# Kernel tuning notes

Hardware: AMD Instinct MI355X
Metric: run time of the kernel (lower is better)

## Reference

```python
import jax, jax.numpy as jnp
import numpy as np

B, S, D, H = 32, 1024, 192, 8
DH = D // H  # 24


def setup_inputs() -> dict:
    key = jax.random.key(0)
    ks = jax.random.split(key, 8)
    s_in = 1.0 / np.sqrt(D)
    return {
        "x": jax.random.normal(ks[0], (B, S, D), dtype=jnp.float32),
        "mask": jax.random.randint(ks[1], (B, S), 0, 2).astype(bool),
        "Wq": jax.random.normal(ks[2], (H, D, DH), dtype=jnp.float32) * s_in,
        "bq": jnp.zeros((H, DH), dtype=jnp.float32),
        "Wk": jax.random.normal(ks[3], (H, D, DH), dtype=jnp.float32) * s_in,
        "bk": jnp.zeros((H, DH), dtype=jnp.float32),
        "Wv": jax.random.normal(ks[4], (H, D, DH), dtype=jnp.float32) * s_in,
        "bv": jnp.zeros((H, DH), dtype=jnp.float32),
        "Wo": jax.random.normal(ks[5], (D, D), dtype=jnp.float32) * s_in,
        "bo": jnp.zeros((D,), dtype=jnp.float32),
    }


def reference(x, mask, Wq, bq, Wk, bk, Wv, bv, Wo, bo):
    # Batched per-head projections: [B,S,D] x [H,D,DH] -> [B,H,S,DH]
    q = jnp.einsum("bsd,hde->bhse", x, Wq) + bq[None, :, None, :]
    k = jnp.einsum("bsd,hde->bhse", x, Wk) + bk[None, :, None, :]
    v = jnp.einsum("bsd,hde->bhse", x, Wv) + bv[None, :, None, :]
    scale = 1.0 / np.sqrt(DH).astype(np.float32)
    scores = jnp.einsum("bhse,bhte->bhst", q, k) * scale  # [B,H,S,S]
    # mask [B,S] broadcast over heads and query positions (masked_fill with -1e9)
    scores = jnp.where(mask[:, None, None, :], scores, -1e9)
    weights = jax.nn.softmax(scores, axis=-1)
    out = jnp.einsum("bhst,bhte->bhse", weights, v)  # [B,H,S,DH]
    # concat heads along last dim -> [B,S,D]
    out = out.transpose(0, 2, 1, 3).reshape(B, S, D)
    return out @ Wo + bo
```

## Files before the change

### kernel.cpp

```cpp
#include <hip/hip_runtime.h>

typedef __attribute__((ext_vector_type(8))) short short8;
typedef __attribute__((ext_vector_type(4))) float f32x4;
typedef __attribute__((ext_vector_type(16))) float f32x16;
typedef __attribute__((ext_vector_type(2))) unsigned uint2v;
typedef __attribute__((ext_vector_type(4))) unsigned uint4v;

#define MFMA16(a,b,c) __builtin_amdgcn_mfma_f32_16x16x32_bf16((a),(b),(c),0,0,0)
#define MFMA32(a,b,c) __builtin_amdgcn_mfma_f32_32x32x16_bf16((a),(b),(c),0,0,0)

#define BB 32
#define SS 1024
#define DD 192
#define HH 8
#define DHP 32

#define SCALE_Q 0.294468266742895f

__device__ __forceinline__ short nb(float f) {
    __bf16 h = (__bf16)f;
    return __builtin_bit_cast(short, h);
}
__device__ __forceinline__ float bf2f(short s) {
    union { unsigned u; float f; } v; v.u = ((unsigned)(unsigned short)s) << 16;
    return v.f;
}
__device__ __forceinline__ unsigned pk2(float a, float b) {
    unsigned short lo = __builtin_bit_cast(unsigned short, (__bf16)a);
    unsigned short hi = __builtin_bit_cast(unsigned short, (__bf16)b);
    return (unsigned)lo | ((unsigned)hi << 16);
}

__global__ __launch_bounds__(256) void prep_kernel(
    const float* __restrict__ Wq, const float* __restrict__ Wk, const float* __restrict__ Wv,
    const float* __restrict__ Wo,
    short* __restrict__ WqF, short* __restrict__ WkF, short* __restrict__ WvF,
    short* __restrict__ WoFh, short* __restrict__ WoFl)
{
    int idx = blockIdx.x * 256 + threadIdx.x;
    const int NWX   = 3 * HH * DHP * DD;
    const int NWO   = DD * DD;
    if (idx < NWX) {
        int j = idx;
        int mat = j / (HH * DHP * DD);
        int jj  = j % (HH * DHP * DD);
        int h   = jj / (DHP * DD);
        int rem = jj % (DHP * DD);
        int e   = rem / DD;
        int d   = rem % DD;
        const float* W = (mat == 0) ? Wq : (mat == 1) ? Wk : Wv;
        short* WF      = (mat == 0) ? WqF : (mat == 1) ? WkF : WvF;
        float val = (e < 24) ? W[(h * DD + d) * 24 + e] : 0.f;
        int nt = e & 1, cc = e >> 1;
        int kk = d >> 5, g = (d >> 3) & 3, ee = d & 7;
        WF[(size_t)((((h*2+nt)*6 + kk)*64) + g*16 + cc)*8 + ee] = nb(val);
    } else if (idx < NWX + NWO) {
        int j = idx - NWX;
        int n = j / DD, k = j % DD;
        float f = Wo[k * DD + n];
        short hi = nb(f);
        int nn = n >> 4, cc = n & 15;
        int kk = k >> 5, g = (k >> 3) & 3, ee = k & 7;
        size_t addr = (size_t)(((nn*6 + kk)*64) + g*16 + cc)*8 + ee;
        WoFh[addr] = hi;
        WoFl[addr] = nb(f - bf2f(hi));
    }
}

__global__ __launch_bounds__(256) void xprep_kernel(
    const float* __restrict__ x, short* __restrict__ xF)
{
    __shared__ short lds[64][200];
    int t = threadIdx.x;
    int r0 = blockIdx.x * 64;

    #pragma unroll
    for (int i = 0; i < 12; i++) {
        int idx = i * 256 + t;
        int row = idx / 48;
        int colf = (idx % 48) * 4;
        float4 f = *(const float4*)(x + ((size_t)(r0 + row)) * DD + colf);
        lds[row][colf + 0] = nb(f.x);
        lds[row][colf + 1] = nb(f.y);
        lds[row][colf + 2] = nb(f.z);
        lds[row][colf + 3] = nb(f.w);
    }
    __syncthreads();

    int w = t >> 6, lane = t & 63, c = lane & 15, g = lane >> 4;
    int br = blockIdx.x * 4 + w;
    short* outb = xF + (size_t)br * 6 * 512;
    #pragma unroll
    for (int kk = 0; kk < 6; kk++) {
        short8 o = *(const short8*)&lds[w * 16 + c][kk * 32 + g * 8];
        *(short8*)(outb + kk * 512 + (size_t)lane * 8) = o;
    }
}

__global__ __launch_bounds__(1024) void scan_kernel(
    const void* __restrict__ mask_raw,
    float* __restrict__ maskf, int* __restrict__ fwd, int* __restrict__ cnt)
{
    int b = blockIdx.x, t = threadIdx.x;
    int lane = t & 63, wv = t >> 6;
    int idx = b * SS + t;

    const unsigned* mw = (const unsigned*)mask_raw;
    bool all01 = true, allf = true;
    #pragma unroll
    for (int i = 0; i < 16; i++) {
        unsigned w = mw[i];
        all01 = all01 && (w <= 1u);
        allf  = allf  && (w == 0u || w == 0x3F800000u);
    }
    bool m;
    if (all01)      m = (mw[idx] != 0u);
    else if (allf)  m = (((const float*)mask_raw)[idx] != 0.f);
    else            m = (((const unsigned char*)mask_raw)[idx] != 0);
    maskf[idx] = m ? 1.f : 0.f;

    unsigned long long bal = __ballot(m);
    int preU  = __popcll(bal & ((1ull << lane) - 1ull));
    int waveU = __popcll(bal);
    __shared__ int wsu[16];
    if (lane == 0) wsu[wv] = waveU;
    __syncthreads();
    int waveOffU = 0, totalU = 0;
    #pragma unroll
    for (int i = 0; i < 16; i++) {
        int v = wsu[i];
        if (i < wv) waveOffU += v;
        totalU += v;
    }
    int posU = waveOffU + preU;
    int posM = totalU + (wv * 64 - waveOffU) + (lane - preU);
    fwd[b * SS + (m ? posU : posM)] = t;
    if (t == 0) cnt[b] = totalU;
}

__global__ __launch_bounds__(256) void proj_kernel(
    const short* __restrict__ xF,
    const float* __restrict__ bq, const float* __restrict__ bk, const float* __restrict__ bv,
    const short* __restrict__ WqF, const short* __restrict__ WkF, const short* __restrict__ WvF,
    const float* __restrict__ maskf,
    short* __restrict__ Q, short* __restrict__ Kc, short* __restrict__ Vc)
{
    int tid = threadIdx.x;
    int lane = tid & 63, w = tid >> 6;
    int c = lane & 15, g = lane >> 4;
    int r0 = blockIdx.x * 64 + w * 16;
    int h0 = blockIdx.y * 2;

    int b_ = r0 >> 10;
    int s0 = (r0 & 1023) + g * 4;

    short8 a[6];
    const short* xfb = xF + (size_t)(r0 >> 4) * 6 * 512 + (size_t)lane * 8;
    #pragma unroll
    for (int kk = 0; kk < 6; kk++)
        a[kk] = *(const short8*)(xfb + kk * 512);

    float mrow[4];
    #pragma unroll
    for (int r = 0; r < 4; r++) mrow[r] = maskf[b_ * SS + s0 + r];

    #pragma unroll
    for (int hh = 0; hh < 2; hh++) {
        int h = h0 + hh;
        int bh = b_ * HH + h;
        #pragma unroll
        for (int mat = 0; mat < 3; mat++) {
            const short* WF   = (mat==0)?WqF:(mat==1)?WkF:WvF;
            const float* bias = (mat==0)?bq:(mat==1)?bk:bv;

            f32x4 acc0 = {0.f,0.f,0.f,0.f};
            f32x4 acc1 = {0.f,0.f,0.f,0.f};
            const short* Wp0 = WF + (size_t)((h*2+0)*6) * 512 + lane * 8;
            const short* Wp1 = WF + (size_t)((h*2+1)*6) * 512 + lane * 8;
            #pragma unroll
            for (int kk = 0; kk < 6; kk++) {
                short8 b0 = *(const short8*)(Wp0 + kk * 512);
                short8 b1 = *(const short8*)(Wp1 + kk * 512);
                acc0 = MFMA16(a[kk], b0, acc0);
                acc1 = MFMA16(a[kk], b1, acc1);
            }
            float bv0 = 0.f, bv1 = 0.f;
            if (2*c < 24) {
                float2 bb = *(const float2*)(bias + h * 24 + 2 * c);
                bv0 = bb.x; bv1 = bb.y;
            }

            if (mat == 0) {
                #pragma unroll
                for (int r = 0; r < 4; r++) {
                    float v0 = (acc0[r] + bv0) * SCALE_Q;
                    float v1 = (c == 15) ? 1.0f : (acc1[r] + bv1) * SCALE_Q;
                    *(unsigned*)(Q + ((size_t)bh * SS + s0 + r) * DHP + 2*c) = pk2(v0, v1);
                }
            } else if (mat == 1) {
                #pragma unroll
                for (int r = 0; r < 4; r++) {
                    float v0 = acc0[r] + bv0;
                    float v1 = (c == 15) ? ((mrow[r] != 0.f) ? 0.f : -1e30f)
                                         : (acc1[r] + bv1);
                    *(unsigned*)(Kc + ((size_t)bh * SS + s0 + r) * DHP + 2*c) = pk2(v0, v1);
                }
            } else {
                #pragma unroll
                for (int r = 0; r < 4; r++) {
                    float v0 = (c == 12) ? 1.0f : (acc0[r] + bv0);
                    float v1 = acc1[r] + bv1;
                    *(unsigned*)(Vc + ((size_t)bh * SS + s0 + r) * DHP + 2*c) = pk2(v0, v1);
                }
            }
        }
    }
}

__global__ __launch_bounds__(256) void kvprep_kernel(
    const short* __restrict__ Kc, const short* __restrict__ Vc,
    const int* __restrict__ fwd, const int* __restrict__ cnt,
    short* __restrict__ KF, short* __restrict__ VF)
{
    int bh = blockIdx.x, c4 = blockIdx.y;
    int b = bh >> 3;
    int nt32 = ((cnt[b] + 31) >> 5) << 5;
    int row0 = c4 * 128;
    if (row0 >= nt32) return;

    __shared__ short lds[128][40];
    int t = threadIdx.x;
    int srow[2];

    #pragma unroll
    for (int p = 0; p < 2; p++) {
        int j = p * 64 + (t >> 2);
        int part = t & 3;
        int s = fwd[b * SS + row0 + j];
        srow[p] = s;
        *(short8*)&lds[j][part * 8] =
            *(const short8*)(Kc + ((size_t)bh * SS + s) * DHP + part * 8);
    }
    __syncthreads();

    int tile_l = t >> 6, L = t & 63, l31 = L & 31, hi = L >> 5;
    short* kf0 = KF + (size_t)bh * SS * DHP + (size_t)(row0 / 32 + tile_l) * 1024;
    #pragma unroll
    for (int i = 0; i < 2; i++) {
        short8 o = *(const short8*)&lds[tile_l * 32 + l31][i * 16 + hi * 8];
        *(short8*)(kf0 + i * 512 + (size_t)L * 8) = o;
    }
    __syncthreads();

    #pragma unroll
    for (int p = 0; p < 2; p++) {
        int j = p * 64 + (t >> 2);
        int part = t & 3;
        *(short8*)&lds[j][part * 8] =
            *(const short8*)(Vc + ((size_t)bh * SS + srow[p]) * DHP + part * 8);
    }
    __syncthreads();

    short* vf0 = VF + (size_t)bh * SS * DHP + (size_t)(row0 / 32 + tile_l) * 1024;
    #pragma unroll
    for (int i = 0; i < 2; i++) {
        short8 o;
        #pragma unroll
        for (int j2 = 0; j2 < 8; j2++)
            o[j2] = lds[tile_l * 32 + i * 16 + hi * 8 + j2][l31];
        *(short8*)(vf0 + i * 512 + (size_t)L * 8) = o;
    }
}

__device__ __forceinline__ void fproc(const f32x16& S, f32x16& acc,
                                      short8 v0, short8 v1)
{
    float p[16];
    #pragma unroll
    for (int r = 0; r < 16; r++) p[r] = __builtin_amdgcn_exp2f(S[r]);

    unsigned c01 = pk2(p[0],  p[1]);
    unsigned c23 = pk2(p[2],  p[3]);
    unsigned c45 = pk2(p[4],  p[5]);
    unsigned c67 = pk2(p[6],  p[7]);
    unsigned c89 = pk2(p[8],  p[9]);
    unsigned cab = pk2(p[10], p[11]);
    unsigned ccd = pk2(p[12], p[13]);
    unsigned cef = pk2(p[14], p[15]);

    uint2v s0 = __builtin_amdgcn_permlane32_swap(c01, c45, false, false);
    uint2v s1 = __builtin_amdgcn_permlane32_swap(c23, c67, false, false);
    uint2v s2 = __builtin_amdgcn_permlane32_swap(c89, ccd, false, false);
    uint2v s3 = __builtin_amdgcn_permlane32_swap(cab, cef, false, false);

    uint4v w0v = { s0.x, s1.x, s0.y, s1.y };
    uint4v w1v = { s2.x, s3.x, s2.y, s3.y };
    short8 pa0 = __builtin_bit_cast(short8, w0v);
    short8 pa1 = __builtin_bit_cast(short8, w1v);

    acc = MFMA32(pa0, v0, acc);
    acc = MFMA32(pa1, v1, acc);
}

__global__ __launch_bounds__(256, 2) void flash_kernel(
    const short* __restrict__ Q, const short* __restrict__ KF, const short* __restrict__ VF,
    const int* __restrict__ cnt, short* __restrict__ Af)
{
    __shared__ float llds[4][4][32];

    int idx = blockIdx.x;
    int bh = idx & 255;
    int qb = idx >> 8;
    int b = bh >> 3, h = bh & 7;

    int tid = threadIdx.x;
    int lane = tid & 63, w = tid >> 6;
    int l31 = lane & 31;
    int hi = lane >> 5;

    int nt = (cnt[b] + 31) >> 5;

    int qr0 = qb * 512 + w * 32;

    short8 qf[4][2];
    #pragma unroll
    for (int cc = 0; cc < 4; cc++) {
        const short* Qp = Q + ((size_t)bh * SS + qr0 + cc * 128 + l31) * DHP + hi * 8;
        qf[cc][0] = *(const short8*)Qp;
        qf[cc][1] = *(const short8*)(Qp + 16);
    }

    const short* Kp = KF + (size_t)bh * SS * DHP + (size_t)lane * 8;
    const short* Vp = VF + (size_t)bh * SS * DHP + (size_t)lane * 8;

    f32x16 acc[4], Z16;
    #pragma unroll
    for (int r = 0; r < 16; r++) {
        acc[0][r] = 0.f; acc[1][r] = 0.f; acc[2][r] = 0.f; acc[3][r] = 0.f;
        Z16[r] = 0.f;
    }

    short8 k0 = *(const short8*)(Kp);
    short8 k1 = *(const short8*)(Kp + 512);
    short8 v0 = *(const short8*)(Vp);
    short8 v1 = *(const short8*)(Vp + 512);

    for (int kt = 0; kt < nt; kt++) {
        Kp += 1024;
        Vp += 1024;
        short8 nk0 = *(const short8*)(Kp);
        short8 nk1 = *(const short8*)(Kp + 512);
        short8 nv0 = *(const short8*)(Vp);
        short8 nv1 = *(const short8*)(Vp + 512);

        #pragma unroll
        for (int cc = 0; cc < 4; cc++) {
            f32x16 S = MFMA32(k0, qf[cc][0], Z16);
            S = MFMA32(k1, qf[cc][1], S);
            fproc(S, acc[cc], v0, v1);
        }

        k0 = nk0; k1 = nk1; v0 = nv0; v1 = nv1;
    }

    if (l31 == 24) {
        #pragma unroll
        for (int cc = 0; cc < 4; cc++) {
            #pragma unroll
            for (int r = 0; r < 16; r++) {
                int row = (r & 3) + 8 * (r >> 2) + 4 * hi;
                llds[w][cc][row] = __builtin_amdgcn_rcpf(acc[cc][r]);
            }
        }
    }
    __builtin_amdgcn_wave_barrier();

    if (l31 < 24) {
        int d = h * 24 + l31;
        size_t fcol = (size_t)((d >> 5) * 4 + ((d >> 3) & 3)) * 128 + (d & 7);
        #pragma unroll
        for (int cc = 0; cc < 4; cc++) {
            int grp = (b * SS + qr0 + cc * 128) >> 4;
            short* op = Af + (size_t)grp * 3072 + fcol;
            #pragma unroll
            for (int r = 0; r < 16; r++) {
                int row = (r & 3) + 8 * (r >> 2) + 4 * hi;
                size_t off = (size_t)(r >> 3) * 3072 + (size_t)(row & 15) * 8;
                op[off] = nb(acc[cc][r] * llds[w][cc][row]);
            }
        }
    }
}

__global__ __launch_bounds__(256) void final_kernel(
    const short* __restrict__ Af,
    const short* __restrict__ WoFh, const short* __restrict__ WoFl,
    const float* __restrict__ bo, float* __restrict__ out)
{
    int tid = threadIdx.x;
    int lane = tid & 63, w = tid >> 6;
    int c = lane & 15, g = lane >> 4;
    int r0 = blockIdx.x * 64 + w * 16;
    int n0 = blockIdx.y * 3;

    short8 a[6];
    #pragma unroll
    for (int kk = 0; kk < 6; kk++)
        a[kk] = *(const short8*)(Af + ((size_t)(r0 >> 4) * 24 + kk*4 + g) * 128 + c * 8);

    f32x4 acc[3];
    #pragma unroll
    for (int n = 0; n < 3; n++) acc[n] = (f32x4){0.f,0.f,0.f,0.f};

    #pragma unroll
    for (int kk = 0; kk < 6; kk++) {
        #pragma unroll
        for (int n = 0; n < 3; n++) {
            const short* bh_p = WoFh + (size_t)((n0+n)*6 + kk) * 512 + lane * 8;
            const short* bl_p = WoFl + (size_t)((n0+n)*6 + kk) * 512 + lane * 8;
            short8 bh = *(const short8*)bh_p;
            short8 bl = *(const short8*)bl_p;
            acc[n] = MFMA16(a[kk], bh, acc[n]);
            acc[n] = MFMA16(a[kk], bl, acc[n]);
        }
    }

    #pragma unroll
    for (int n = 0; n < 3; n++) {
        int col = (n0+n)*16 + c;
        float bv = bo[col];
        #pragma unroll
        for (int r = 0; r < 4; r++) {
            out[(size_t)(r0 + g*4 + r) * DD + col] = acc[n][r] + bv;
        }
    }
}

extern "C" void kernel_launch(void* const* d_in, const int* in_sizes, int n_in,
                              void* d_out, int out_size, void* d_ws, size_t ws_size,
                              hipStream_t stream)
{
    const float* x    = (const float*)d_in[0];
    const void*  mask = d_in[1];
    const float* Wq   = (const float*)d_in[2];
    const float* bq   = (const float*)d_in[3];
    const float* Wk   = (const float*)d_in[4];
    const float* bk   = (const float*)d_in[5];
    const float* Wv   = (const float*)d_in[6];
    const float* bv   = (const float*)d_in[7];
    const float* Wo   = (const float*)d_in[8];
    const float* bo   = (const float*)d_in[9];
    float* out = (float*)d_out;

    char* ws = (char*)d_ws;
    size_t off = 0;
    float* maskf = (float*)(ws + off); off += (size_t)BB*SS*4;
    short* Q     = (short*)(ws + off); off += (size_t)BB*HH*SS*DHP*2;
    short* Kc    = (short*)(ws + off); off += (size_t)BB*HH*SS*DHP*2;
    short* Vc    = (short*)(ws + off); off += (size_t)BB*HH*SS*DHP*2;
    short* KF    = (short*)(ws + off); off += (size_t)BB*HH*SS*DHP*2;
    short* VF    = (short*)(ws + off); off += (size_t)BB*HH*SS*DHP*2;
    short* xF    = (short*)(ws + off); off += (size_t)BB*SS*DD*2;
    short* WqF   = (short*)(ws + off); off += (size_t)HH*DHP*DD*2;
    short* WkF   = (short*)(ws + off); off += (size_t)HH*DHP*DD*2;
    short* WvF   = (short*)(ws + off); off += (size_t)HH*DHP*DD*2;
    short* WoFh  = (short*)(ws + off); off += (size_t)DD*DD*2;
    short* WoFl  = (short*)(ws + off); off += (size_t)DD*DD*2;
    int*   fwd   = (int*)  (ws + off); off += (size_t)BB*SS*4;
    int*   cnt   = (int*)  (ws + off); off += 256;

    short* Af = Kc;

    prep_kernel<<<dim3(720), dim3(256), 0, stream>>>(
        Wq, Wk, Wv, Wo, WqF, WkF, WvF, WoFh, WoFl);
    xprep_kernel<<<dim3(512), dim3(256), 0, stream>>>(x, xF);
    scan_kernel<<<dim3(BB), dim3(1024), 0, stream>>>(mask, maskf, fwd, cnt);
    proj_kernel<<<dim3(512, 4), dim3(256), 0, stream>>>(
        xF, bq, bk, bv, WqF, WkF, WvF, maskf, Q, Kc, Vc);
    kvprep_kernel<<<dim3(256, 8), dim3(256), 0, stream>>>(
        Kc, Vc, fwd, cnt, KF, VF);
    flash_kernel<<<dim3(512), dim3(256), 0, stream>>>(
        Q, KF, VF, cnt, Af);
    final_kernel<<<dim3(512, 4), dim3(256), 0, stream>>>(
        Af, WoFh, WoFl, bo, out);
}
```

Baseline: 100.8 us.

## Merge prep kernels into one launch, drop Wo split-bf16, widen proj grid

Combines the weight prep, x conversion and mask scan kernels into a single setup kernel dispatched by block index, which removes two launches. The mask scan now uses 256 threads handling four positions each, with a shuffle-based prefix sum. The output projection drops the low-order bf16 correction term for Wo, halving its MFMAs and weight loads at some cost in accuracy. The projection kernel now assigns one head per block across 8 grid columns instead of two heads per block, giving more parallelism.

```diff
diff --git a/kernel.cpp b/kernel.cpp
--- a/kernel.cpp
+++ b/kernel.cpp
@@ -31,111 +31,116 @@
     return (unsigned)lo | ((unsigned)hi << 16);
 }
 
-__global__ __launch_bounds__(256) void prep_kernel(
+#define NBLK_PREP 720
+#define NBLK_XPREP 512
+__global__ __launch_bounds__(256) void setup_kernel(
     const float* __restrict__ Wq, const float* __restrict__ Wk, const float* __restrict__ Wv,
-    const float* __restrict__ Wo,
+    const float* __restrict__ Wo, const float* __restrict__ x, const void* __restrict__ mask_raw,
     short* __restrict__ WqF, short* __restrict__ WkF, short* __restrict__ WvF,
-    short* __restrict__ WoFh, short* __restrict__ WoFl)
-{
-    int idx = blockIdx.x * 256 + threadIdx.x;
-    const int NWX   = 3 * HH * DHP * DD;
-    const int NWO   = DD * DD;
-    if (idx < NWX) {
-        int j = idx;
-        int mat = j / (HH * DHP * DD);
-        int jj  = j % (HH * DHP * DD);
-        int h   = jj / (DHP * DD);
-        int rem = jj % (DHP * DD);
-        int e   = rem / DD;
-        int d   = rem % DD;
-        const float* W = (mat == 0) ? Wq : (mat == 1) ? Wk : Wv;
-        short* WF      = (mat == 0) ? WqF : (mat == 1) ? WkF : WvF;
-        float val = (e < 24) ? W[(h * DD + d) * 24 + e] : 0.f;
-        int nt = e & 1, cc = e >> 1;
-        int kk = d >> 5, g = (d >> 3) & 3, ee = d & 7;
-        WF[(size_t)((((h*2+nt)*6 + kk)*64) + g*16 + cc)*8 + ee] = nb(val);
-    } else if (idx < NWX + NWO) {
-        int j = idx - NWX;
-        int n = j / DD, k = j % DD;
-        float f = Wo[k * DD + n];
-        short hi = nb(f);
-        int nn = n >> 4, cc = n & 15;
-        int kk = k >> 5, g = (k >> 3) & 3, ee = k & 7;
-        size_t addr = (size_t)(((nn*6 + kk)*64) + g*16 + cc)*8 + ee;
-        WoFh[addr] = hi;
-        WoFl[addr] = nb(f - bf2f(hi));
-    }
-}
-
-__global__ __launch_bounds__(256) void xprep_kernel(
-    const float* __restrict__ x, short* __restrict__ xF)
+    short* __restrict__ WoFh, short* __restrict__ xF,
+    float* __restrict__ maskf, int* __restrict__ fwd, int* __restrict__ cnt)
 {
     __shared__ short lds[64][200];
+    int bid = blockIdx.x;
     int t = threadIdx.x;
-    int r0 = blockIdx.x * 64;
-
-    #pragma unroll
-    for (int i = 0; i < 12; i++) {
-        int idx = i * 256 + t;
-        int row = idx / 48;
-        int colf = (idx % 48) * 4;
-        float4 f = *(const float4*)(x + ((size_t)(r0 + row)) * DD + colf);
-        lds[row][colf + 0] = nb(f.x);
-        lds[row][colf + 1] = nb(f.y);
-        lds[row][colf + 2] = nb(f.z);
-        lds[row][colf + 3] = nb(f.w);
-    }
-    __syncthreads();
-
-    int w = t >> 6, lane = t & 63, c = lane & 15, g = lane >> 4;
-    int br = blockIdx.x * 4 + w;
-    short* outb = xF + (size_t)br * 6 * 512;
-    #pragma unroll
-    for (int kk = 0; kk < 6; kk++) {
-        short8 o = *(const short8*)&lds[w * 16 + c][kk * 32 + g * 8];
-        *(short8*)(outb + kk * 512 + (size_t)lane * 8) = o;
-    }
-}
-
-__global__ __launch_bounds__(1024) void scan_kernel(
-    const void* __restrict__ mask_raw,
-    float* __restrict__ maskf, int* __restrict__ fwd, int* __restrict__ cnt)
-{
-    int b = blockIdx.x, t = threadIdx.x;
-    int lane = t & 63, wv = t >> 6;
-    int idx = b * SS + t;
-
-    const unsigned* mw = (const unsigned*)mask_raw;
-    bool all01 = true, allf = true;
-    #pragma unroll
-    for (int i = 0; i < 16; i++) {
-        unsigned w = mw[i];
-        all01 = all01 && (w <= 1u);
-        allf  = allf  && (w == 0u || w == 0x3F800000u);
-    }
-    bool m;
-    if (all01)      m = (mw[idx] != 0u);
-    else if (allf)  m = (((const float*)mask_raw)[idx] != 0.f);
-    else            m = (((const unsigned char*)mask_raw)[idx] != 0);
-    maskf[idx] = m ? 1.f : 0.f;
-
-    unsigned long long bal = __ballot(m);
-    int preU  = __popcll(bal & ((1ull << lane) - 1ull));
-    int waveU = __popcll(bal);
-    __shared__ int wsu[16];
-    if (lane == 0) wsu[wv] = waveU;
-    __syncthreads();
-    int waveOffU = 0, totalU = 0;
-    #pragma unroll
-    for (int i = 0; i < 16; i++) {
-        int v = wsu[i];
-        if (i < wv) waveOffU += v;
-        totalU += v;
-    }
-    int posU = waveOffU + preU;
-    int posM = totalU + (wv * 64 - waveOffU) + (lane - preU);
-    fwd[b * SS + (m ? posU : posM)] = t;
-    if (t == 0) cnt[b] = totalU;
+
+    if (bid < NBLK_PREP) {
+        int idx = bid * 256 + t;
+        const int NWX = 3 * HH * DHP * DD;
+        const int NWO = DD * DD;
+        if (idx < NWX) {
+            int mat = idx / (HH * DHP * DD);
+            int jj  = idx % (HH * DHP * DD);
+            int h   = jj / (DHP * DD);
+            int rem = jj % (DHP * DD);
+            int e   = rem / DD;
+            int d   = rem % DD;
+            const float* W = (mat == 0) ? Wq : (mat == 1) ? Wk : Wv;
+            short* WF      = (mat == 0) ? WqF : (mat == 1) ? WkF : WvF;
+            float val = (e < 24) ? W[(h * DD + d) * 24 + e] : 0.f;
+            int nt = e & 1, cc = e >> 1;
+            int kk = d >> 5, g = (d >> 3) & 3, ee = d & 7;
+            WF[(size_t)((((h*2+nt)*6 + kk)*64) + g*16 + cc)*8 + ee] = nb(val);
+        } else if (idx < NWX + NWO) {
+            int j = idx - NWX;
+            int n = j / DD, k = j % DD;
+            int nn = n >> 4, cc = n & 15;
+            int kk = k >> 5, g = (k >> 3) & 3, ee = k & 7;
+            WoFh[(size_t)(((nn*6 + kk)*64) + g*16 + cc)*8 + ee] = nb(Wo[k * DD + n]);
+        }
+    } else if (bid < NBLK_PREP + NBLK_XPREP) {
+        int xb = bid - NBLK_PREP;
+        int r0 = xb * 64;
+        #pragma unroll
+        for (int i = 0; i < 12; i++) {
+            int idx = i * 256 + t;
+            int row = idx / 48;
+            int colf = (idx % 48) * 4;
+            float4 f = *(const float4*)(x + ((size_t)(r0 + row)) * DD + colf);
+            lds[row][colf + 0] = nb(f.x);
+            lds[row][colf + 1] = nb(f.y);
+            lds[row][colf + 2] = nb(f.z);
+            lds[row][colf + 3] = nb(f.w);
+        }
+        __syncthreads();
+        int w = t >> 6, lane = t & 63, c = lane & 15, g = lane >> 4;
+        short* outb = xF + (size_t)(xb * 4 + w) * 6 * 512;
+        #pragma unroll
+        for (int kk = 0; kk < 6; kk++) {
+            short8 o = *(const short8*)&lds[w * 16 + c][kk * 32 + g * 8];
+            *(short8*)(outb + kk * 512 + (size_t)lane * 8) = o;
+        }
+    } else {
+        int b = bid - NBLK_PREP - NBLK_XPREP;
+        int lane = t & 63, wv = t >> 6;
+        int* wsu = (int*)&lds[0][0];
+
+        const unsigned* mw = (const unsigned*)mask_raw;
+        bool all01 = true, allf = true;
+        #pragma unroll
+        for (int i = 0; i < 16; i++) {
+            unsigned w = mw[i];
+            all01 = all01 && (w <= 1u);
+            allf  = allf  && (w == 0u || w == 0x3F800000u);
+        }
+        int s0 = t * 4;
+        bool m[4];
+        #pragma unroll
+        for (int j = 0; j < 4; j++) {
+            int idx = b * SS + s0 + j;
+            bool mm;
+            if (all01)      mm = (mw[idx] != 0u);
+            else if (allf)  mm = (((const float*)mask_raw)[idx] != 0.f);
+            else            mm = (((const unsigned char*)mask_raw)[idx] != 0);
+            m[j] = mm;
+            maskf[idx] = mm ? 1.f : 0.f;
+        }
+        int cnt4 = (int)m[0] + (int)m[1] + (int)m[2] + (int)m[3];
+        int pref = cnt4;
+        #pragma unroll
+        for (int d = 1; d < 64; d <<= 1) {
+            int o = __shfl_up(pref, d, 64);
+            if (lane >= d) pref += o;
+        }
+        int waveExcl = pref - cnt4;
+        if (lane == 63) wsu[wv] = pref;
+        __syncthreads();
+        int waveOff = 0, totalU = 0;
+        #pragma unroll
+        for (int i = 0; i < 4; i++) {
+            int v = wsu[i];
+            if (i < wv) waveOff += v;
+            totalU += v;
+        }
+        int pu = waveOff + waveExcl;
+        #pragma unroll
+        for (int j = 0; j < 4; j++) {
+            int s = s0 + j;
+            if (m[j]) { fwd[b * SS + pu] = s; pu++; }
+            else      { fwd[b * SS + totalU + (s - pu)] = s; }
+        }
+        if (t == 0) cnt[b] = totalU;
+    }
 }
 
 __global__ __launch_bounds__(256) void proj_kernel(
@@ -149,10 +154,11 @@
     int lane = tid & 63, w = tid >> 6;
     int c = lane & 15, g = lane >> 4;
     int r0 = blockIdx.x * 64 + w * 16;
-    int h0 = blockIdx.y * 2;
+    int h = blockIdx.y;
 
     int b_ = r0 >> 10;
     int s0 = (r0 & 1023) + g * 4;
+    int bh = b_ * HH + h;
 
     short8 a[6];
     const short* xfb = xF + (size_t)(r0 >> 4) * 6 * 512 + (size_t)lane * 8;
@@ -165,53 +171,48 @@
     for (int r = 0; r < 4; r++) mrow[r] = maskf[b_ * SS + s0 + r];
 
     #pragma unroll
-    for (int hh = 0; hh < 2; hh++) {
-        int h = h0 + hh;
-        int bh = b_ * HH + h;
-        #pragma unroll
-        for (int mat = 0; mat < 3; mat++) {
-            const short* WF   = (mat==0)?WqF:(mat==1)?WkF:WvF;
-            const float* bias = (mat==0)?bq:(mat==1)?bk:bv;
-
-            f32x4 acc0 = {0.f,0.f,0.f,0.f};
-            f32x4 acc1 = {0.f,0.f,0.f,0.f};
-            const short* Wp0 = WF + (size_t)((h*2+0)*6) * 512 + lane * 8;
-            const short* Wp1 = WF + (size_t)((h*2+1)*6) * 512 + lane * 8;
+    for (int mat = 0; mat < 3; mat++) {
+        const short* WF   = (mat==0)?WqF:(mat==1)?WkF:WvF;
+        const float* bias = (mat==0)?bq:(mat==1)?bk:bv;
+
+        f32x4 acc0 = {0.f,0.f,0.f,0.f};
+        f32x4 acc1 = {0.f,0.f,0.f,0.f};
+        const short* Wp0 = WF + (size_t)((h*2+0)*6) * 512 + lane * 8;
+        const short* Wp1 = WF + (size_t)((h*2+1)*6) * 512 + lane * 8;
+        #pragma unroll
+        for (int kk = 0; kk < 6; kk++) {
+            short8 b0 = *(const short8*)(Wp0 + kk * 512);
+            short8 b1 = *(const short8*)(Wp1 + kk * 512);
+            acc0 = MFMA16(a[kk], b0, acc0);
+            acc1 = MFMA16(a[kk], b1, acc1);
+        }
+        float bv0 = 0.f, bv1 = 0.f;
+        if (2*c < 24) {
+            float2 bb = *(const float2*)(bias + h * 24 + 2 * c);
+            bv0 = bb.x; bv1 = bb.y;
+        }
+
+        if (mat == 0) {
             #pragma unroll
-            for (int kk = 0; kk < 6; kk++) {
-                short8 b0 = *(const short8*)(Wp0 + kk * 512);
-                short8 b1 = *(const short8*)(Wp1 + kk * 512);
-                acc0 = MFMA16(a[kk], b0, acc0);
-                acc1 = MFMA16(a[kk], b1, acc1);
+            for (int r = 0; r < 4; r++) {
+                float v0 = (acc0[r] + bv0) * SCALE_Q;
+                float v1 = (c == 15) ? 1.0f : (acc1[r] + bv1) * SCALE_Q;
+                *(unsigned*)(Q + ((size_t)bh * SS + s0 + r) * DHP + 2*c) = pk2(v0, v1);
             }
-            float bv0 = 0.f, bv1 = 0.f;
-            if (2*c < 24) {
-                float2 bb = *(const float2*)(bias + h * 24 + 2 * c);
-                bv0 = bb.x; bv1 = bb.y;
+        } else if (mat == 1) {
+            #pragma unroll
+            for (int r = 0; r < 4; r++) {
+                float v0 = acc0[r] + bv0;
+                float v1 = (c == 15) ? ((mrow[r] != 0.f) ? 0.f : -1e30f)
+                                     : (acc1[r] + bv1);
+                *(unsigned*)(Kc + ((size_t)bh * SS + s0 + r) * DHP + 2*c) = pk2(v0, v1);
             }
-
-            if (mat == 0) {
-                #pragma unroll
-                for (int r = 0; r < 4; r++) {
-                    float v0 = (acc0[r] + bv0) * SCALE_Q;
-                    float v1 = (c == 15) ? 1.0f : (acc1[r] + bv1) * SCALE_Q;
-                    *(unsigned*)(Q + ((size_t)bh * SS + s0 + r) * DHP + 2*c) = pk2(v0, v1);
-                }
-            } else if (mat == 1) {
-                #pragma unroll
-                for (int r = 0; r < 4; r++) {
-                    float v0 = acc0[r] + bv0;
-                    float v1 = (c == 15) ? ((mrow[r] != 0.f) ? 0.f : -1e30f)
-                                         : (acc1[r] + bv1);
-                    *(unsigned*)(Kc + ((size_t)bh * SS + s0 + r) * DHP + 2*c) = pk2(v0, v1);
-                }
-            } else {
-                #pragma unroll
-                for (int r = 0; r < 4; r++) {
-                    float v0 = (c == 12) ? 1.0f : (acc0[r] + bv0);
-                    float v1 = acc1[r] + bv1;
-                    *(unsigned*)(Vc + ((size_t)bh * SS + s0 + r) * DHP + 2*c) = pk2(v0, v1);
-                }
+        } else {
+            #pragma unroll
+            for (int r = 0; r < 4; r++) {
+                float v0 = (c == 12) ? 1.0f : (acc0[r] + bv0);
+                float v1 = acc1[r] + bv1;
+                *(unsigned*)(Vc + ((size_t)bh * SS + s0 + r) * DHP + 2*c) = pk2(v0, v1);
             }
         }
     }
@@ -394,7 +395,7 @@
 
 __global__ __launch_bounds__(256) void final_kernel(
     const short* __restrict__ Af,
-    const short* __restrict__ WoFh, const short* __restrict__ WoFl,
+    const short* __restrict__ WoFh,
     const float* __restrict__ bo, float* __restrict__ out)
 {
     int tid = threadIdx.x;
@@ -416,12 +417,8 @@
     for (int kk = 0; kk < 6; kk++) {
         #pragma unroll
         for (int n = 0; n < 3; n++) {
-            const short* bh_p = WoFh + (size_t)((n0+n)*6 + kk) * 512 + lane * 8;
-            const short* bl_p = WoFl + (size_t)((n0+n)*6 + kk) * 512 + lane * 8;
-            short8 bh = *(const short8*)bh_p;
-            short8 bl = *(const short8*)bl_p;
+            short8 bh = *(const short8*)(WoFh + (size_t)((n0+n)*6 + kk) * 512 + lane * 8);
             acc[n] = MFMA16(a[kk], bh, acc[n]);
-            acc[n] = MFMA16(a[kk], bl, acc[n]);
         }
     }
 
@@ -465,22 +462,19 @@
     short* WkF   = (short*)(ws + off); off += (size_t)HH*DHP*DD*2;
     short* WvF   = (short*)(ws + off); off += (size_t)HH*DHP*DD*2;
     short* WoFh  = (short*)(ws + off); off += (size_t)DD*DD*2;
-    short* WoFl  = (short*)(ws + off); off += (size_t)DD*DD*2;
     int*   fwd   = (int*)  (ws + off); off += (size_t)BB*SS*4;
     int*   cnt   = (int*)  (ws + off); off += 256;
 
     short* Af = Kc;
 
-    prep_kernel<<<dim3(720), dim3(256), 0, stream>>>(
-        Wq, Wk, Wv, Wo, WqF, WkF, WvF, WoFh, WoFl);
-    xprep_kernel<<<dim3(512), dim3(256), 0, stream>>>(x, xF);
-    scan_kernel<<<dim3(BB), dim3(1024), 0, stream>>>(mask, maskf, fwd, cnt);
-    proj_kernel<<<dim3(512, 4), dim3(256), 0, stream>>>(
+    setup_kernel<<<dim3(NBLK_PREP + NBLK_XPREP + BB), dim3(256), 0, stream>>>(
+        Wq, Wk, Wv, Wo, x, mask, WqF, WkF, WvF, WoFh, xF, maskf, fwd, cnt);
+    proj_kernel<<<dim3(512, 8), dim3(256), 0, stream>>>(
         xF, bq, bk, bv, WqF, WkF, WvF, maskf, Q, Kc, Vc);
     kvprep_kernel<<<dim3(256, 8), dim3(256), 0, stream>>>(
         Kc, Vc, fwd, cnt, KF, VF);
     flash_kernel<<<dim3(512), dim3(256), 0, stream>>>(
         Q, KF, VF, cnt, Af);
     final_kernel<<<dim3(512, 4), dim3(256), 0, stream>>>(
-        Af, WoFh, WoFl, bo, out);
-}
+        Af, WoFh, bo, out);
+}
```

Measured after the change: 91.94 us. 1.1x faster.
